# Kernel optimization log

Hardware: AMD Instinct MI355X
Metric: run time of the kernel (lower is better)

The kernel has to match this reference:

```python
import jax, jax.numpy as jnp
import numpy as np

BSZ, L, D = 64, 128, 2048


def setup_inputs() -> dict:
    key = jax.random.key(0)
    k1, k2, k3 = jax.random.split(key, 3)
    encoder_output = jax.random.normal(k1, (BSZ, L, D), dtype=jnp.float32)
    # ragged turn lengths in [2, L]; prefix mask like torch turn_lengths = mask.sum(1)
    lengths = jax.random.randint(k2, (BSZ,), 2, L + 1)
    mask = (jnp.arange(L)[None, :] < lengths[:, None]).astype(jnp.int32)
    W = jax.random.normal(k3, (2 * D, 2), dtype=jnp.float32) * (1.0 / np.sqrt(2 * D))
    b = jnp.zeros((2,), dtype=jnp.float32)
    return {"encoder_output": encoder_output, "mask": mask, "W": W, "b": b}


def reference(encoder_output, mask, W, b):
    bsz, max_len, d = encoder_output.shape
    turn_lengths = jnp.sum(mask, axis=1)  # [bsz]
    # con_fc(concat(h_j, h_k)) == h_j @ W[:d] + h_k @ W[d:] + b  (exact split of the linear)
    left = jnp.einsum('bld,dc->blc', encoder_output, W[:d])   # [b, L, 2]
    right = jnp.einsum('bld,dc->blc', encoder_output, W[d:])  # [b, L, 2]
    logits = left[:, :, None, :] + right[:, None, :, :] + b   # [b, L(j), L(k), 2]
    j = jnp.arange(max_len)[:, None]
    k = jnp.arange(max_len)[None, :]
    # pairs gathered by torch loops: k < j < turn_lengths[i]; label 1 iff k == j-1
    valid = (k < j) & (j < turn_lengths[:, None, None])        # [b, L, L]
    labels = (k == j - 1).astype(jnp.int32)                    # [L, L]
    logp = jax.nn.log_softmax(logits, axis=-1)                 # [b, L, L, 2]
    nll = -jnp.take_along_axis(
        logp, jnp.broadcast_to(labels[None, :, :, None], (bsz, max_len, max_len, 1)), axis=-1
    )[..., 0]                                                  # [b, L, L]
    n_valid = jnp.sum(valid)
    dli_loss = jnp.sum(jnp.where(valid, nll, 0.0)) / jnp.maximum(n_valid, 1).astype(nll.dtype)
    return dli_loss
```

## Files before the change

kernel.cpp:

```cpp
#include <hip/hip_runtime.h>

#define BSZ 64
#define LMAX 128
#define DIM 2048
#define NPOS (BSZ * LMAX)

struct Ctrl {
    float accum;
    int   count;
    int   done2;
};

__global__ __launch_bounds__(512, 4) void proj_kernel(
        const float* __restrict__ enc,
        const float* __restrict__ W,
        float* __restrict__ proj,
        Ctrl* __restrict__ ctrl) {
    if (blockIdx.x == 0 && threadIdx.x == 0) {
        ctrl->accum = 0.f; ctrl->count = 0; ctrl->done2 = 0;
    }

    const int tid  = threadIdx.x;
    const int wid  = tid >> 6;
    const int lane = tid & 63;
    const int pair = wid >> 1;
    const int half = wid & 1;
    const int p0   = blockIdx.x * 16 + pair * 4;

    const float4* __restrict__ W4 = (const float4*)W;
    float4 wl0[4], wl1[4], wr0[4], wr1[4];
    #pragma unroll
    for (int it = 0; it < 4; ++it) {
        const int idx = half * 256 + it * 64 + lane;
        wl0[it] = W4[idx * 2];
        wl1[it] = W4[idx * 2 + 1];
        wr0[it] = W4[1024 + idx * 2];
        wr1[it] = W4[1024 + idx * 2 + 1];
    }

    float a0[4], a1[4], a2[4], a3[4];
    #pragma unroll
    for (int q = 0; q < 4; ++q) { a0[q] = a1[q] = a2[q] = a3[q] = 0.f; }

    const float4* __restrict__ h4 = (const float4*)enc;
    const size_t base = (size_t)p0 * (DIM / 4) + half * 256 + lane;

    float4 hq[4];
    #pragma unroll
    for (int it = 0; it < 4; ++it) hq[it] = h4[base + it * 64];

    #pragma unroll
    for (int q = 0; q < 4; ++q) {
        float4 hn[4];
        if (q < 3) {
            #pragma unroll
            for (int it = 0; it < 4; ++it)
                hn[it] = h4[base + (size_t)(q + 1) * (DIM / 4) + it * 64];
        }
        #pragma unroll
        for (int it = 0; it < 4; ++it) {
            const float4 h = hq[it];
            a0[q] += h.x * wl0[it].x + h.y * wl0[it].z + h.z * wl1[it].x + h.w * wl1[it].z;
            a1[q] += h.x * wl0[it].y + h.y * wl0[it].w + h.z * wl1[it].y + h.w * wl1[it].w;
            a2[q] += h.x * wr0[it].x + h.y * wr0[it].z + h.z * wr1[it].x + h.w * wr1[it].z;
            a3[q] += h.x * wr0[it].y + h.y * wr0[it].w + h.z * wr1[it].y + h.w * wr1[it].w;
        }
        if (q < 3) {
            #pragma unroll
            for (int it = 0; it < 4; ++it) hq[it] = hn[it];
        }
    }

    float* __restrict__ projf = proj + (size_t)half * NPOS * 4;
    #pragma unroll
    for (int q = 0; q < 4; ++q) {
        const bool o1 = (lane & 1);
        const float r1 = __shfl_xor(o1 ? a0[q] : a1[q], 1);
        float s = (o1 ? a1[q] : a0[q]) + r1;
        const float r2 = __shfl_xor(o1 ? a2[q] : a3[q], 1);
        float t = (o1 ? a3[q] : a2[q]) + r2;
        const bool o2 = (lane & 2);
        const float r3 = __shfl_xor(o2 ? s : t, 2);
        float u = (o2 ? t : s) + r3;
        u += __shfl_xor(u, 4);
        u += __shfl_xor(u, 8);
        u += __shfl_xor(u, 16);
        u += __shfl_xor(u, 32);
        if (lane < 4) projf[(size_t)(p0 + q) * 4 + lane] = u;
    }
}

__global__ __launch_bounds__(256) void loss_kernel(
        const int* __restrict__ mask,
        const float* __restrict__ proj,
        const float* __restrict__ bias,
        Ctrl* __restrict__ ctrl,
        float* __restrict__ out) {
    __shared__ float4 s_proj[LMAX];
    __shared__ float  s_w[4];
    __shared__ int    s_m[4];

    const int b   = blockIdx.x >> 2;
    const int q   = blockIdx.x & 3;
    const int tid = threadIdx.x;

    const float4* proj4 = (const float4*)proj;
    if (tid < LMAX) {
        const float4 pa = proj4[b * LMAX + tid];
        const float4 pb = proj4[NPOS + b * LMAX + tid];
        float4 v;
        v.x = pa.x + pb.x; v.y = pa.y + pb.y;
        v.z = pa.z + pb.z; v.w = pa.w + pb.w;
        s_proj[tid] = v;
    }

    int m = (tid < LMAX) ? mask[b * LMAX + tid] : 0;
    #pragma unroll
    for (int off = 32; off >= 1; off >>= 1) m += __shfl_xor(m, off);
    if ((tid & 63) == 0) s_m[tid >> 6] = m;
    __syncthreads();

    const int   T  = s_m[0] + s_m[1] + s_m[2] + s_m[3];
    const float b0 = bias[0];
    const float b1 = bias[1];

    float local = 0.f;
    const int tmax = T << 7;
    for (int t = q * 256 + tid; t < tmax; t += 1024) {
        const int j = t >> 7;
        const int k = t & (LMAX - 1);
        if (k < j) {
            const float4 pj = s_proj[j];
            const float4 pk = s_proj[k];
            const float l0 = pj.x + pk.z + b0;
            const float l1 = pj.y + pk.w + b1;
            const bool  pos = (k == j - 1);
            const float d  = pos ? (l0 - l1) : (l1 - l0);
            local += fmaxf(d, 0.f) + __logf(1.f + __expf(-fabsf(d)));
        }
    }

    #pragma unroll
    for (int off = 32; off >= 1; off >>= 1) local += __shfl_xor(local, off);
    if ((tid & 63) == 0) s_w[tid >> 6] = local;
    __syncthreads();

    if (tid == 0) {
        atomicAdd(&ctrl->accum, s_w[0] + s_w[1] + s_w[2] + s_w[3]);
        if (q == 0) atomicAdd(&ctrl->count, T * (T - 1) / 2);
        __threadfence();
        const int prev = atomicAdd(&ctrl->done2, 1);
        if (prev == 4 * BSZ - 1) {
            const float s = atomicAdd(&ctrl->accum, 0.0f);
            const int   c = atomicAdd(&ctrl->count, 0);
            out[0] = s / (float)(c > 1 ? c : 1);
        }
    }
}

extern "C" void kernel_launch(void* const* d_in, const int* in_sizes, int n_in,
                              void* d_out, int out_size, void* d_ws, size_t ws_size,
                              hipStream_t stream) {
    const float* enc  = (const float*)d_in[0];
    const int*   mask = (const int*)d_in[1];
    const float* W    = (const float*)d_in[2];
    const float* bias = (const float*)d_in[3];
    float* out = (float*)d_out;

    float* proj = (float*)d_ws;
    Ctrl*  ctrl = (Ctrl*)((char*)d_ws + 2 * NPOS * 16);

    proj_kernel<<<NPOS / 16, 512, 0, stream>>>(enc, W, proj, ctrl);
    loss_kernel<<<4 * BSZ, 256, 0, stream>>>(mask, proj, bias, ctrl, out);
}
```

Baseline: 27.42 us.

## Split projection dot products four ways per position to raise occupancy

The projection kernel now splits each position's 2048-wide dot product across four waves instead of two. Each wave holds half as many weight and activation registers, which allows a higher launch-bounds occupancy hint, and the grid doubles so twice as many blocks stream the encoder tensor. The loss kernel now sums four partial projection buffers instead of two, so the workspace and partial-sum traffic grow. The aim is more memory-level parallelism on a bandwidth-bound read of 64 MB.

```diff
diff --git a/kernel.cpp b/kernel.cpp
--- a/kernel.cpp
+++ b/kernel.cpp
@@ -11,7 +11,7 @@
     int   done2;
 };
 
-__global__ __launch_bounds__(512, 4) void proj_kernel(
+__global__ __launch_bounds__(512, 6) void proj_kernel(
         const float* __restrict__ enc,
         const float* __restrict__ W,
         float* __restrict__ proj,
@@ -23,62 +23,52 @@
     const int tid  = threadIdx.x;
     const int wid  = tid >> 6;
     const int lane = tid & 63;
-    const int pair = wid >> 1;
-    const int half = wid & 1;
-    const int p0   = blockIdx.x * 16 + pair * 4;
+    const int quad = wid >> 2;
+    const int qw   = wid & 3;
+    const int p0   = (blockIdx.x * 2 + quad) * 4;
 
     const float4* __restrict__ W4 = (const float4*)W;
-    float4 wl0[4], wl1[4], wr0[4], wr1[4];
+    float4 wl0[2], wl1[2], wr0[2], wr1[2];
     #pragma unroll
-    for (int it = 0; it < 4; ++it) {
-        const int idx = half * 256 + it * 64 + lane;
+    for (int it = 0; it < 2; ++it) {
+        const int idx = qw * 128 + it * 64 + lane;
         wl0[it] = W4[idx * 2];
         wl1[it] = W4[idx * 2 + 1];
         wr0[it] = W4[1024 + idx * 2];
         wr1[it] = W4[1024 + idx * 2 + 1];
     }
 
-    float a0[4], a1[4], a2[4], a3[4];
-    #pragma unroll
-    for (int q = 0; q < 4; ++q) { a0[q] = a1[q] = a2[q] = a3[q] = 0.f; }
+    const float4* __restrict__ h4 = (const float4*)enc;
+    const size_t base = (size_t)p0 * (DIM / 4) + qw * 128 + lane;
 
-    const float4* __restrict__ h4 = (const float4*)enc;
-    const size_t base = (size_t)p0 * (DIM / 4) + half * 256 + lane;
+    float4 hA0 = h4[base];
+    float4 hA1 = h4[base + 64];
 
-    float4 hq[4];
-    #pragma unroll
-    for (int it = 0; it < 4; ++it) hq[it] = h4[base + it * 64];
+    float* __restrict__ projf = proj + (size_t)qw * NPOS * 4;
 
     #pragma unroll
     for (int q = 0; q < 4; ++q) {
-        float4 hn[4];
+        float4 hB0, hB1;
         if (q < 3) {
-            #pragma unroll
-            for (int it = 0; it < 4; ++it)
-                hn[it] = h4[base + (size_t)(q + 1) * (DIM / 4) + it * 64];
+            const size_t nb = base + (size_t)(q + 1) * (DIM / 4);
+            hB0 = h4[nb];
+            hB1 = h4[nb + 64];
         }
-        #pragma unroll
-        for (int it = 0; it < 4; ++it) {
-            const float4 h = hq[it];
-            a0[q] += h.x * wl0[it].x + h.y * wl0[it].z + h.z * wl1[it].x + h.w * wl1[it].z;
-            a1[q] += h.x * wl0[it].y + h.y * wl0[it].w + h.z * wl1[it].y + h.w * wl1[it].w;
-            a2[q] += h.x * wr0[it].x + h.y * wr0[it].z + h.z * wr1[it].x + h.w * wr1[it].z;
-            a3[q] += h.x * wr0[it].y + h.y * wr0[it].w + h.z * wr1[it].y + h.w * wr1[it].w;
-        }
-        if (q < 3) {
-            #pragma unroll
-            for (int it = 0; it < 4; ++it) hq[it] = hn[it];
-        }
-    }
+        float a0, a1, a2, a3;
+        a0 = hA0.x * wl0[0].x + hA0.y * wl0[0].z + hA0.z * wl1[0].x + hA0.w * wl1[0].z
+           + hA1.x * wl0[1].x + hA1.y * wl0[1].z + hA1.z * wl1[1].x + hA1.w * wl1[1].z;
+        a1 = hA0.x * wl0[0].y + hA0.y * wl0[0].w + hA0.z * wl1[0].y + hA0.w * wl1[0].w
+           + hA1.x * wl0[1].y + hA1.y * wl0[1].w + hA1.z * wl1[1].y + hA1.w * wl1[1].w;
+        a2 = hA0.x * wr0[0].x + hA0.y * wr0[0].z + hA0.z * wr1[0].x + hA0.w * wr1[0].z
+           + hA1.x * wr0[1].x + hA1.y * wr0[1].z + hA1.z * wr1[1].x + hA1.w * wr1[1].z;
+        a3 = hA0.x * wr0[0].y + hA0.y * wr0[0].w + hA0.z * wr1[0].y + hA0.w * wr1[0].w
+           + hA1.x * wr0[1].y + hA1.y * wr0[1].w + hA1.z * wr1[1].y + hA1.w * wr1[1].w;
 
-    float* __restrict__ projf = proj + (size_t)half * NPOS * 4;
-    #pragma unroll
-    for (int q = 0; q < 4; ++q) {
         const bool o1 = (lane & 1);
-        const float r1 = __shfl_xor(o1 ? a0[q] : a1[q], 1);
-        float s = (o1 ? a1[q] : a0[q]) + r1;
-        const float r2 = __shfl_xor(o1 ? a2[q] : a3[q], 1);
-        float t = (o1 ? a3[q] : a2[q]) + r2;
+        const float r1 = __shfl_xor(o1 ? a0 : a1, 1);
+        float s = (o1 ? a1 : a0) + r1;
+        const float r2 = __shfl_xor(o1 ? a2 : a3, 1);
+        float t = (o1 ? a3 : a2) + r2;
         const bool o2 = (lane & 2);
         const float r3 = __shfl_xor(o2 ? s : t, 2);
         float u = (o2 ? t : s) + r3;
@@ -87,6 +77,8 @@
         u += __shfl_xor(u, 16);
         u += __shfl_xor(u, 32);
         if (lane < 4) projf[(size_t)(p0 + q) * 4 + lane] = u;
+
+        if (q < 3) { hA0 = hB0; hA1 = hB1; }
     }
 }
 
@@ -106,11 +98,15 @@
 
     const float4* proj4 = (const float4*)proj;
     if (tid < LMAX) {
-        const float4 pa = proj4[b * LMAX + tid];
-        const float4 pb = proj4[NPOS + b * LMAX + tid];
+        const float4 pa = proj4[0 * NPOS + b * LMAX + tid];
+        const float4 pb = proj4[1 * NPOS + b * LMAX + tid];
+        const float4 pc = proj4[2 * NPOS + b * LMAX + tid];
+        const float4 pd = proj4[3 * NPOS + b * LMAX + tid];
         float4 v;
-        v.x = pa.x + pb.x; v.y = pa.y + pb.y;
-        v.z = pa.z + pb.z; v.w = pa.w + pb.w;
+        v.x = (pa.x + pb.x) + (pc.x + pd.x);
+        v.y = (pa.y + pb.y) + (pc.y + pd.y);
+        v.z = (pa.z + pb.z) + (pc.z + pd.z);
+        v.w = (pa.w + pb.w) + (pc.w + pd.w);
         s_proj[tid] = v;
     }
 
@@ -168,8 +164,8 @@
     float* out = (float*)d_out;
 
     float* proj = (float*)d_ws;
-    Ctrl*  ctrl = (Ctrl*)((char*)d_ws + 2 * NPOS * 16);
+    Ctrl*  ctrl = (Ctrl*)((char*)d_ws + 4 * NPOS * 16);
 
-    proj_kernel<<<NPOS / 16, 512, 0, stream>>>(enc, W, proj, ctrl);
+    proj_kernel<<<NPOS / 8, 512, 0, stream>>>(enc, W, proj, ctrl);
     loss_kernel<<<4 * BSZ, 256, 0, stream>>>(mask, proj, bias, ctrl, out);
 }
```

New measurement: 26.93 us. About the same (-1.8%).
